# Optimization experiments

Hardware: AMD Instinct MI355X
Metric: run time of the kernel (lower is better)

The kernel has to match this reference:

```python
import jax, jax.numpy as jnp
import numpy as np

D_MODEL = 1024
D_STATE = 256

def setup_inputs() -> dict:
    key = jax.random.key(0)
    k1, k2, k3, k4 = jax.random.split(key, 4)
    x = jax.random.normal(k1, (8, 4096, D_MODEL), dtype=jnp.float32)
    A = jax.random.normal(k2, (D_STATE,), dtype=jnp.float32)
    B = jax.random.normal(k3, (D_STATE, D_MODEL), dtype=jnp.float32) * 0.01
    C = jax.random.normal(k4, (D_MODEL, D_STATE), dtype=jnp.float32) * 0.01
    D = jnp.ones((D_MODEL,), dtype=jnp.float32)
    return {"x": x, "A": A, "B": B, "C": C, "D": D}

def reference(x, A, B, C, D):
    # x: (b, s, d_model)
    a_bar = jnp.exp(-jnp.exp(A))                     # (n,)
    Bx = jnp.einsum('bsd,nd->bsn', x, B)             # (b, s, n) precomputed input drive

    def step(h, bx_t):
        h = a_bar * h + bx_t                          # (b, n)
        return h, h

    h0 = jnp.zeros((x.shape[0], A.shape[0]), dtype=x.dtype)
    # scan over time axis: move seq to leading axis
    _, hs = jax.lax.scan(step, h0, jnp.swapaxes(Bx, 0, 1))  # hs: (s, b, n)
    hs = jnp.swapaxes(hs, 0, 1)                      # (b, s, n)
    y = jnp.einsum('bsn,dn->bsd', hs, C) + D * x     # (b, s, d_model)
    return y
```

## Files before the change

kernel.cpp:

```cpp
#include <hip/hip_runtime.h>
#include <cstdint>
#include <cstddef>


typedef __attribute__((ext_vector_type(8))) _Float16 half8;
typedef __attribute__((ext_vector_type(4))) float f32x4;

__device__ inline half8 cvt8(float4 a, float4 b) {
  half8 h;
  h[0] = (_Float16)a.x; h[1] = (_Float16)a.y;
  h[2] = (_Float16)a.z; h[3] = (_Float16)a.w;
  h[4] = (_Float16)b.x; h[5] = (_Float16)b.y;
  h[6] = (_Float16)b.z; h[7] = (_Float16)b.w;
  return h;
}

__global__ __launch_bounds__(256) void cvt_bc(
    const float* __restrict__ Bp, const float* __restrict__ Cp,
    _Float16* __restrict__ Bh, _Float16* __restrict__ Ch)
{
  const int g = blockIdx.x * 256 + threadIdx.x;
  const size_t off = (size_t)(g & 32767) * 8;
  const float* src = (g < 32768) ? (Bp + off) : (Cp + off);
  _Float16*    dst = (g < 32768) ? (Bh + off) : (Ch + off);
  float4 a = *(const float4*)src;
  float4 b = *(const float4*)(src + 4);
  *(half8*)dst = cvt8(a, b);
}

__global__ __launch_bounds__(256) void gemm_bx(
    const float* __restrict__ x, const _Float16* __restrict__ Bh,
    const float* __restrict__ Ap,
    _Float16* __restrict__ Bxh, float* __restrict__ E)
{
  __shared__ _Float16 lb[256 * 128];

  const int tid  = threadIdx.x;
  const int lane = tid & 63;
  const int wave = tid >> 6;
  const int quad = lane >> 4;
  const int l16  = lane & 15;
  const long blockM = (long)blockIdx.x * 64;
  const long arow = blockM + wave * 16 + l16;

  f32x4 acc[16];
  #pragma unroll
  for (int i = 0; i < 16; i++) acc[i] = (f32x4){0.f, 0.f, 0.f, 0.f};

  for (int kc = 0; kc < 8; kc++) {
    __syncthreads();
    {
      const int n = tid;
      const _Float16* src = Bh + (size_t)n * 1024 + kc * 128;
      #pragma unroll
      for (int j = 0; j < 16; j++) {
        half8 v = *(const half8*)(src + j * 8);
        const int k8p = j ^ (n & 7);
        *(half8*)&lb[n * 128 + k8p * 8] = v;
      }
    }
    half8 af[4];
    #pragma unroll
    for (int ks = 0; ks < 4; ks++) {
      const float* ga = x + arow * 1024 + kc * 128 + ks * 32 + quad * 8;
      float4 a0 = *(const float4*)ga;
      float4 a1 = *(const float4*)(ga + 4);
      af[ks] = cvt8(a0, a1);
    }
    __syncthreads();
    #pragma unroll
    for (int ks = 0; ks < 4; ks++) {
      #pragma unroll
      for (int nt = 0; nt < 16; nt++) {
        const int n   = nt * 16 + l16;
        const int k8p = (ks * 4 + quad) ^ (n & 7);
        half8 bf = *(const half8*)&lb[n * 128 + k8p * 8];
        acc[nt] = __builtin_amdgcn_mfma_f32_16x16x32_f16(af[ks], bf, acc[nt], 0, 0, 0);
      }
    }
  }

  __syncthreads();
  #pragma unroll
  for (int nt = 0; nt < 16; nt++)
    #pragma unroll
    for (int r = 0; r < 4; r++)
      lb[(wave * 16 + quad * 4 + r) * 256 + nt * 16 + l16] = (_Float16)acc[nt][r];
  __syncthreads();
  {
    const int row = tid >> 2, seg = tid & 3;
    _Float16* dst = Bxh + (blockM + row) * 256 + seg * 64;
    const _Float16* srcl = &lb[row * 256 + seg * 64];
    #pragma unroll
    for (int j = 0; j < 8; j++)
      *(half8*)(dst + j * 8) = *(const half8*)(srcl + j * 8);
  }
  {
    const float al = expf(-expf(Ap[tid]));
    float h = 0.f;
    #pragma unroll 8
    for (int t = 0; t < 64; t++)
      h = fmaf(al, h, (float)lb[t * 256 + tid]);
    E[(size_t)blockIdx.x * 256 + tid] = h;
  }
}

__global__ __launch_bounds__(256) void scan_prefix(
    const float* __restrict__ E, const float* __restrict__ Ap,
    float* __restrict__ carry)
{
  __shared__ float4 se4[4096];
  const int n = threadIdx.x;
  const int b = blockIdx.x;

  const float4* src4 = (const float4*)(E + (size_t)b * 64 * 256);
  #pragma unroll
  for (int j = 0; j < 16; j++)
    se4[j * 256 + n] = src4[j * 256 + n];

  const float al = expf(-expf(Ap[n]));
  float aL = al;
  #pragma unroll
  for (int i = 0; i < 6; i++) aL *= aL;

  __syncthreads();
  const float* se = (const float*)se4;
  float run = 0.f;
  for (int c = 0; c < 64; c++) {
    carry[((size_t)b * 64 + c) * 256 + n] = run;
    run = fmaf(aL, run, se[c * 256 + n]);
  }
}

__global__ __launch_bounds__(256) void scan_apply(
    _Float16* __restrict__ Bxh, const float* __restrict__ Ap,
    const float* __restrict__ carry)
{
  const int n  = threadIdx.x;
  const int bc = blockIdx.x;
  const float al = expf(-expf(Ap[n]));
  float h = carry[(size_t)bc * 256 + n];
  const size_t base = (size_t)bc * 64 * 256 + n;
  #pragma unroll 16
  for (int t = 0; t < 64; t++) {
    const size_t i = base + (size_t)t * 256;
    h = fmaf(al, h, (float)Bxh[i]);
    Bxh[i] = (_Float16)h;
  }
}

__global__ __launch_bounds__(256, 4) void gemm_y(
    const _Float16* __restrict__ hs, const _Float16* __restrict__ Ch,
    const float* __restrict__ x, const float* __restrict__ Dp,
    float* __restrict__ y)
{
  __shared__ _Float16 lc[64 * 256];

  const int tid  = threadIdx.x;
  const int lane = tid & 63;
  const int wave = tid >> 6;
  const int quad = lane >> 4;
  const int l16  = lane & 15;
  const int cg   = blockIdx.x & 1;
  const long mg  = blockIdx.x >> 1;
  const long row = mg * 64 + wave * 16 + l16;

  half8 af[8];
  {
    const _Float16* ph = hs + row * 256;
    #pragma unroll
    for (int ks = 0; ks < 8; ks++)
      af[ks] = *(const half8*)(ph + ks * 32 + quad * 8);
  }

  const int nfill = tid >> 2, qfill = tid & 3;

  for (int it = 0; it < 8; it++) {
    const int n0 = cg * 512 + it * 64;

    if (it) __syncthreads();
    {
      const _Float16* src = Ch + (size_t)(n0 + nfill) * 256 + qfill * 64;
      #pragma unroll
      for (int j = 0; j < 8; j++) {
        half8 v = *(const half8*)(src + j * 8);
        const int k8p = (qfill * 8 + j) ^ (nfill & 7);
        *(half8*)&lc[nfill * 256 + k8p * 8] = v;
      }
    }

    const float* px = x + row * 1024 + n0 + quad * 4;
    const float* pD = Dp + n0 + quad * 4;
    float4 xv[4], dv[4];
    #pragma unroll
    for (int nt = 0; nt < 4; nt++) {
      xv[nt] = *(const float4*)(px + nt * 16);
      dv[nt] = *(const float4*)(pD + nt * 16);
    }

    __syncthreads();

    f32x4 acc[4];
    #pragma unroll
    for (int nt = 0; nt < 4; nt++) acc[nt] = (f32x4){0.f, 0.f, 0.f, 0.f};

    #pragma unroll
    for (int ks = 0; ks < 8; ks++) {
      #pragma unroll
      for (int nt = 0; nt < 4; nt++) {
        const int nl  = nt * 16 + l16;
        const int k8p = (ks * 4 + quad) ^ (nl & 7);
        half8 cf = *(const half8*)&lc[nl * 256 + k8p * 8];
        acc[nt] = __builtin_amdgcn_mfma_f32_16x16x32_f16(cf, af[ks], acc[nt], 0, 0, 0);
      }
    }

    float* py = y + row * 1024 + n0 + quad * 4;
    #pragma unroll
    for (int nt = 0; nt < 4; nt++) {
      float4 o;
      o.x = acc[nt][0] + dv[nt].x * xv[nt].x;
      o.y = acc[nt][1] + dv[nt].y * xv[nt].y;
      o.z = acc[nt][2] + dv[nt].z * xv[nt].z;
      o.w = acc[nt][3] + dv[nt].w * xv[nt].w;
      *(float4*)(py + nt * 16) = o;
    }
  }
}

extern "C" void kernel_launch(void* const* d_in, const int* in_sizes, int n_in,
                              void* d_out, int out_size, void* d_ws, size_t ws_size,
                              hipStream_t stream) {
  const float* x  = (const float*)d_in[0];
  const float* Ap = (const float*)d_in[1];
  const float* Bp = (const float*)d_in[2];
  const float* Cp = (const float*)d_in[3];
  const float* Dp = (const float*)d_in[4];
  float* y = (float*)d_out;

  _Float16* Bxh = (_Float16*)d_ws;
  _Float16* Bh  = Bxh + (size_t)32768 * 256;
  _Float16* Ch  = Bh + (size_t)256 * 1024;
  float* E      = (float*)(Ch + (size_t)1024 * 256);
  float* carry  = E + (size_t)512 * 256;

  cvt_bc     <<<256,  256, 0, stream>>>(Bp, Cp, Bh, Ch);
  gemm_bx    <<<512,  256, 0, stream>>>(x, Bh, Ap, Bxh, E);
  scan_prefix<<<8,    256, 0, stream>>>(E, Ap, carry);
  scan_apply <<<512,  256, 0, stream>>>(Bxh, Ap, carry);
  gemm_y     <<<1024, 256, 0, stream>>>(Bxh, Ch, x, Dp, y);
}
```

Measured before the change: 323.1 us.

## Fuse scan apply into output GEMM via LDS-resident chunk, read C from global

Removes the separate scan_apply kernel. Each gemm_y block loads its 64-row chunk of Bx into LDS, applies the carried recurrence in place, and takes its MFMA A-fragments from LDS. This avoids one read and one write of the full Bx buffer in global memory and one launch. C fragments are now read straight from global (L2-cached) instead of being staged through LDS, which drops per-iteration barriers but adds global load latency inside the MFMA loop. Each chunk's scan is also computed twice, once by each of the two column-group blocks.

```diff
diff --git a/kernel.cpp b/kernel.cpp
--- a/kernel.cpp
+++ b/kernel.cpp
@@ -132,29 +132,13 @@
   }
 }
 
-__global__ __launch_bounds__(256) void scan_apply(
-    _Float16* __restrict__ Bxh, const float* __restrict__ Ap,
-    const float* __restrict__ carry)
-{
-  const int n  = threadIdx.x;
-  const int bc = blockIdx.x;
-  const float al = expf(-expf(Ap[n]));
-  float h = carry[(size_t)bc * 256 + n];
-  const size_t base = (size_t)bc * 64 * 256 + n;
-  #pragma unroll 16
-  for (int t = 0; t < 64; t++) {
-    const size_t i = base + (size_t)t * 256;
-    h = fmaf(al, h, (float)Bxh[i]);
-    Bxh[i] = (_Float16)h;
-  }
-}
-
-__global__ __launch_bounds__(256, 4) void gemm_y(
-    const _Float16* __restrict__ hs, const _Float16* __restrict__ Ch,
+__global__ __launch_bounds__(256, 4) void gemm_y_scan(
+    const _Float16* __restrict__ Bxh, const _Float16* __restrict__ Ch,
     const float* __restrict__ x, const float* __restrict__ Dp,
+    const float* __restrict__ Ap, const float* __restrict__ carry,
     float* __restrict__ y)
 {
-  __shared__ _Float16 lc[64 * 256];
+  __shared__ _Float16 lb[64 * 256];
 
   const int tid  = threadIdx.x;
   const int lane = tid & 63;
@@ -163,42 +147,54 @@
   const int l16  = lane & 15;
   const int cg   = blockIdx.x & 1;
   const long mg  = blockIdx.x >> 1;
+
+  {
+    const _Float16* src = Bxh + mg * 64 * 256;
+    #pragma unroll
+    for (int p = 0; p < 8; p++) {
+      half8 v = *(const half8*)(src + p * 2048 + tid * 8);
+      const int r   = p * 8 + (tid >> 5);
+      const int k8p = (tid & 31) ^ (r & 7);
+      *(half8*)&lb[r * 256 + k8p * 8] = v;
+    }
+  }
+  __syncthreads();
+
+  {
+    const float al = expf(-expf(Ap[tid]));
+    float h = carry[mg * 256 + tid];
+    const int k8 = tid >> 3, e = tid & 7;
+    #pragma unroll 8
+    for (int t = 0; t < 64; t++) {
+      const int idx = t * 256 + ((k8 ^ (t & 7)) * 8 + e);
+      h = fmaf(al, h, (float)lb[idx]);
+      lb[idx] = (_Float16)h;
+    }
+  }
+  __syncthreads();
+
   const long row = mg * 64 + wave * 16 + l16;
-
   half8 af[8];
   {
-    const _Float16* ph = hs + row * 256;
-    #pragma unroll
-    for (int ks = 0; ks < 8; ks++)
-      af[ks] = *(const half8*)(ph + ks * 32 + quad * 8);
-  }
-
-  const int nfill = tid >> 2, qfill = tid & 3;
-
+    const int r = wave * 16 + l16;
+    #pragma unroll
+    for (int ks = 0; ks < 8; ks++) {
+      const int k8p = (ks * 4 + quad) ^ (r & 7);
+      af[ks] = *(const half8*)&lb[r * 256 + k8p * 8];
+    }
+  }
+
+  const float* px = x + row * 1024;
+  float*       py = y + row * 1024;
   for (int it = 0; it < 8; it++) {
     const int n0 = cg * 512 + it * 64;
 
-    if (it) __syncthreads();
-    {
-      const _Float16* src = Ch + (size_t)(n0 + nfill) * 256 + qfill * 64;
-      #pragma unroll
-      for (int j = 0; j < 8; j++) {
-        half8 v = *(const half8*)(src + j * 8);
-        const int k8p = (qfill * 8 + j) ^ (nfill & 7);
-        *(half8*)&lc[nfill * 256 + k8p * 8] = v;
-      }
-    }
-
-    const float* px = x + row * 1024 + n0 + quad * 4;
-    const float* pD = Dp + n0 + quad * 4;
     float4 xv[4], dv[4];
     #pragma unroll
     for (int nt = 0; nt < 4; nt++) {
-      xv[nt] = *(const float4*)(px + nt * 16);
-      dv[nt] = *(const float4*)(pD + nt * 16);
-    }
-
-    __syncthreads();
+      xv[nt] = *(const float4*)(px + n0 + nt * 16 + quad * 4);
+      dv[nt] = *(const float4*)(Dp + n0 + nt * 16 + quad * 4);
+    }
 
     f32x4 acc[4];
     #pragma unroll
@@ -208,14 +204,12 @@
     for (int ks = 0; ks < 8; ks++) {
       #pragma unroll
       for (int nt = 0; nt < 4; nt++) {
-        const int nl  = nt * 16 + l16;
-        const int k8p = (ks * 4 + quad) ^ (nl & 7);
-        half8 cf = *(const half8*)&lc[nl * 256 + k8p * 8];
+        const half8 cf = *(const half8*)(
+            Ch + (size_t)(n0 + nt * 16 + l16) * 256 + ks * 32 + quad * 8);
         acc[nt] = __builtin_amdgcn_mfma_f32_16x16x32_f16(cf, af[ks], acc[nt], 0, 0, 0);
       }
     }
 
-    float* py = y + row * 1024 + n0 + quad * 4;
     #pragma unroll
     for (int nt = 0; nt < 4; nt++) {
       float4 o;
@@ -223,7 +217,7 @@
       o.y = acc[nt][1] + dv[nt].y * xv[nt].y;
       o.z = acc[nt][2] + dv[nt].z * xv[nt].z;
       o.w = acc[nt][3] + dv[nt].w * xv[nt].w;
-      *(float4*)(py + nt * 16) = o;
+      *(float4*)(py + n0 + nt * 16 + quad * 4) = o;
     }
   }
 }
@@ -247,6 +241,5 @@
   cvt_bc     <<<256,  256, 0, stream>>>(Bp, Cp, Bh, Ch);
   gemm_bx    <<<512,  256, 0, stream>>>(x, Bh, Ap, Bxh, E);
   scan_prefix<<<8,    256, 0, stream>>>(E, Ap, carry);
-  scan_apply <<<512,  256, 0, stream>>>(Bxh, Ap, carry);
-  gemm_y     <<<1024, 256, 0, stream>>>(Bxh, Ch, x, Dp, y);
-}
+  gemm_y_scan<<<1024, 256, 0, stream>>>(Bxh, Ch, x, Dp, Ap, carry, y);
+}
```

Measured after the change: 418.2 us. 1.29x slower.
